# Kernel tuning notes

Hardware: AMD Instinct MI355X
Metric: run time of the kernel (lower is better)

Reference implementation:

```python
import jax, jax.numpy as jnp
import numpy as np

D = 256; HD = 16; G = 16; L = 2; HOP = 2; HK = 4
N = 16384; E = 49152; B = 256
VA = 128; VB = 8
SQRT2PI = float(np.sqrt(2.0 * 3.14159))  # module uses pi=3.14159


def group_norm(x, g=G, eps=1e-5):
    # torch GroupNorm(affine=False) on [N, D, 1]: normalize over each group of D//g channels
    n, d = x.shape
    xg = x.reshape(n, g, d // g)
    m = xg.mean(-1, keepdims=True)
    v = ((xg - m) ** 2).mean(-1, keepdims=True)
    return ((xg - m) * jax.lax.rsqrt(v + eps)).reshape(n, d)


def glin(x, w):
    # grouped 1x1 conv (no bias): x [n, g*din], w [g, dout, din] -> [n, g*dout]
    g, dout, din = w.shape
    return jnp.einsum('ngd,god->ngo', x.reshape(-1, g, din), w).reshape(-1, g * dout)


def multi_embed(idx, tables):
    # OGB-style encoder: sum of per-feature embeddings. idx [M,F], tables [F,V,D]
    out = tables[0][idx[:, 0]]
    for f in range(1, tables.shape[0]):
        out = out + tables[f][idx[:, f]]
    return out


def glb(x, pre_w, pre_b, gate_w, val_w, post_w, post_b):
    # GatedLinearBlock (dropout is identity in eval)
    xx = group_norm(x @ pre_w.T + pre_b)
    xx = jax.nn.relu(glin(xx, gate_w)) * glin(xx, val_w)
    return xx @ post_w.T + post_b


def glb2(xg, xv, gate_w, val_w, post_w, post_b):
    # GatedLinearBlock2: separate gate/value inputs, GroupNorm first
    gg = jax.nn.relu(glin(group_norm(xg), gate_w))
    vv = glin(group_norm(xv), val_w)
    return (gg * vv) @ post_w.T + post_b


def forward_impl(x_feat, edge_index, edge_attr, batch, batch_size,
                 edge_distance, atom_emb, bond2d_emb, gauss_means, gauss_stds,
                 attn_w, attn_b, scale_both,
                 conv_bond_emb, conv_pre_w, conv_gate_w, conv_val_w, conv_post_w, conv_post_b, conv_scale,
                 virt_pre_w, virt_pre_b, virt_gate_w, virt_val_w, virt_post_w, virt_post_b, virt_scale,
                 att_pre_w, att_pre_b, att_q_w, att_k_w, att_v_w, att_post_w, att_post_b, att_scale,
                 main_pre_w, main_pre_b, main_gate_w, main_val_w, main_post_w, main_post_b):
    src, dst = edge_index[0], edge_index[1]
    n = x_feat.shape[0]
    deg = jnp.clip(jax.ops.segment_sum(jnp.ones_like(dst), dst, num_segments=n) - 1, 0, 3)
    # --- edge features, mode='both': fuse 2D bond embedding with 3D gaussian features ---
    h2d = multi_embed(edge_attr, bond2d_emb)                      # [E, D]
    std = jnp.abs(gauss_stds) + 0.01
    diff = (edge_distance[:, None] - gauss_means[None, :]) / std
    h3d = jnp.exp(-0.5 * diff * diff) / (SQRT2PI * std)          # [E, D]
    w = jax.nn.sigmoid(jnp.concatenate([h2d, h3d], axis=-1) @ attn_w + attn_b[0])[:, None]
    h_e = w * h2d + (1.0 - w) * h3d
    h_in = jnp.exp(scale_both)[deg] * jax.ops.segment_sum(h_e, dst, num_segments=n)
    h_in = multi_embed(x_feat, atom_emb) + h_in                   # [N, D]
    h_virt = jnp.zeros((batch_size, D), h_in.dtype)
    h_att = jnp.zeros((batch_size, 2 * D // HD, HD, HD), h_in.dtype)
    for l in range(L):
        # --- ConvMessage: hop*kernel gated message-passing sublayers ---
        x_raw, x_out = h_in, jnp.zeros_like(h_in)
        for k in range(HK):
            if k > 0 and k % HOP == 0:
                x_raw, x_out = h_in + x_out, jnp.zeros_like(h_in)
            bond = multi_embed(edge_attr, conv_bond_emb[l, k])
            xp = x_raw @ conv_pre_w[l, k].T
            msg = glb2(xp[dst] + bond, xp[src] + bond,
                       conv_gate_w[l, k], conv_val_w[l, k], conv_post_w[l, k], conv_post_b[l, k])
            x_raw = jax.ops.segment_sum(msg, dst, num_segments=n)
            x_out = x_out + jnp.exp(conv_scale[l, k])[deg] * x_raw
        h_out = h_in + x_out
        # --- VirtMessage: graph-level virtual node with residual state ---
        h_virt = jax.ops.segment_sum(h_in, batch, num_segments=batch_size) + h_virt
        h_out = h_out + (jnp.exp(virt_scale[l]) * glb(h_virt, virt_pre_w[l], virt_pre_b[l],
                          virt_gate_w[l], virt_val_w[l], virt_post_w[l], virt_post_b[l]))[batch]
        # --- AttMessage: linear attention with per-graph scatter normalization ---
        xv0 = group_norm(h_in @ att_pre_w[l].T + att_pre_b[l])
        xq = jnp.exp(glin(xv0, att_q_w[l]) / np.sqrt(HD)).reshape(n, -1, HD)   # [N,32,16]
        xk = jnp.exp(glin(xv0, att_k_w[l]) / np.sqrt(HD)).reshape(n, -1, HD)
        xv = glin(xv0, att_v_w[l]).reshape(n, -1, HD)
        xkv = jnp.einsum('bnh,bnv->bnhv', xk, xv)                               # [N,32,16,16]
        h_att = jax.ops.segment_sum(xkv, batch, num_segments=batch_size) + h_att
        xk_sum = jax.ops.segment_sum(xk, batch, num_segments=batch_size)[batch]
        xq = xq / jnp.einsum('bnh,bnh->bn', xq, xk_sum)[:, :, None]
        att_out = jnp.einsum('bnh,bnhv->bnv', xq, h_att[batch]).reshape(n, 2 * D)
        h_out = h_out + jnp.exp(att_scale[l]) * (att_out @ att_post_w[l].T + att_post_b[l])
        # --- main gated block ---
        h_in = glb(h_out, main_pre_w[l], main_pre_b[l],
                   main_gate_w[l], main_val_w[l], main_post_w[l], main_post_b[l])
    return h_in


def setup_inputs() -> dict:
    key = jax.random.key(0)
    ks = iter(jax.random.split(key, 80))
    def rn(shape, s=0.05):
        return jax.random.normal(next(ks), shape, dtype=jnp.float32) * s
    inp = {}
    inp['x_feat'] = jax.random.randint(next(ks), (N, 9), 0, VA)
    inp['edge_index'] = jax.random.randint(next(ks), (2, E), 0, N)
    inp['edge_attr'] = jax.random.randint(next(ks), (E, 3), 0, VB)
    inp['batch'] = jnp.sort(jax.random.randint(next(ks), (N,), 0, B))
    inp['batch_size'] = B
    inp['edge_distance'] = jax.random.uniform(next(ks), (E,), dtype=jnp.float32) * 4.0
    inp['atom_emb'] = rn((9, VA, D))
    inp['bond2d_emb'] = rn((3, VB, D))
    inp['gauss_means'] = jax.random.uniform(next(ks), (D,), minval=2.0, maxval=3.0)
    inp['gauss_stds'] = jax.random.uniform(next(ks), (D,), minval=1.0, maxval=1.5)
    inp['attn_w'] = rn((2 * D,))
    inp['attn_b'] = rn((1,))
    inp['scale_both'] = jnp.full((4, D), np.log(0.1), jnp.float32)
    inp['conv_bond_emb'] = rn((L, HK, 3, VB, D))
    inp['conv_pre_w'] = rn((L, HK, D, D))
    inp['conv_gate_w'] = rn((L, HK, G, HD, HD))
    inp['conv_val_w'] = rn((L, HK, G, HD, HD))
    inp['conv_post_w'] = rn((L, HK, D, D))
    inp['conv_post_b'] = rn((L, HK, D))
    inp['conv_scale'] = jnp.full((L, HK, 4, D), np.log(0.1), jnp.float32)
    inp['virt_pre_w'] = rn((L, D, D)); inp['virt_pre_b'] = rn((L, D))
    inp['virt_gate_w'] = rn((L, G, 2 * HD, HD)); inp['virt_val_w'] = rn((L, G, 2 * HD, HD))
    inp['virt_post_w'] = rn((L, D, 2 * D)); inp['virt_post_b'] = rn((L, D))
    inp['virt_scale'] = jnp.full((L, D), np.log(0.01), jnp.float32)
    inp['att_pre_w'] = rn((L, D, D)); inp['att_pre_b'] = rn((L, D))
    inp['att_q_w'] = rn((L, G, 2 * HD, HD)); inp['att_k_w'] = rn((L, G, 2 * HD, HD)); inp['att_v_w'] = rn((L, G, 2 * HD, HD))
    inp['att_post_w'] = rn((L, D, 2 * D)); inp['att_post_b'] = rn((L, D))
    inp['att_scale'] = jnp.full((L, D), np.log(0.01), jnp.float32)
    inp['main_pre_w'] = rn((L, D, D)); inp['main_pre_b'] = rn((L, D))
    inp['main_gate_w'] = rn((L, G, 3 * HD, HD)); inp['main_val_w'] = rn((L, G, 3 * HD, HD))
    inp['main_post_w'] = rn((L, D, 3 * D)); inp['main_post_b'] = rn((L, D))
    return inp


def reference(x_feat, edge_index, edge_attr, batch, batch_size, edge_distance,
              atom_emb, bond2d_emb, gauss_means, gauss_stds, attn_w, attn_b, scale_both,
              conv_bond_emb, conv_pre_w, conv_gate_w, conv_val_w, conv_post_w, conv_post_b, conv_scale,
              virt_pre_w, virt_pre_b, virt_gate_w, virt_val_w, virt_post_w, virt_post_b, virt_scale,
              att_pre_w, att_pre_b, att_q_w, att_k_w, att_v_w, att_post_w, att_post_b, att_scale,
              main_pre_w, main_pre_b, main_gate_w, main_val_w, main_post_w, main_post_b):
    return forward_impl(x_feat, edge_index, edge_attr, batch, batch_size,
                        edge_distance, atom_emb, bond2d_emb, gauss_means, gauss_stds,
                        attn_w, attn_b, scale_both,
                        conv_bond_emb, conv_pre_w, conv_gate_w, conv_val_w, conv_post_w, conv_post_b, conv_scale,
                        virt_pre_w, virt_pre_b, virt_gate_w, virt_val_w, virt_post_w, virt_post_b, virt_scale,
                        att_pre_w, att_pre_b, att_q_w, att_k_w, att_v_w, att_post_w, att_post_b, att_scale,
                        main_pre_w, main_pre_b, main_gate_w, main_val_w, main_post_w, main_post_b)
```

## Files before the change

### kernel.cpp

```cpp
#include <hip/hip_runtime.h>
#include <cstdint>
#include <cstddef>
#include <type_traits>

#define NN 16384
#define EE 49152
#define BB 256

typedef _Float16 f16;
typedef _Float16 half8 __attribute__((ext_vector_type(8)));
typedef _Float16 half4v __attribute__((ext_vector_type(4)));
typedef _Float16 half2v __attribute__((ext_vector_type(2)));
typedef float floatx4 __attribute__((ext_vector_type(4)));

#if defined(__has_builtin)
#if __has_builtin(__builtin_amdgcn_fdot2)
#define HAVE_FDOT2 1
#endif
#endif

static constexpr size_t ND = (size_t)NN * 256;


__global__ __launch_bounds__(256) void count_deg_kernel(const int* __restrict__ dst, int* __restrict__ cnt, int e) {
  int i = blockIdx.x * 256 + threadIdx.x;
  if (i < e) atomicAdd(&cnt[dst[i]], 1);
}
__global__ __launch_bounds__(256) void clip_deg_kernel(const int* __restrict__ cnt, int* __restrict__ deg, int n) {
  int i = blockIdx.x * 256 + threadIdx.x;
  if (i < n) { int v = cnt[i] - 1; deg[i] = v < 0 ? 0 : (v > 3 ? 3 : v); }
}
__global__ __launch_bounds__(256) void goff_kernel(const int* __restrict__ batch, int* __restrict__ goff, int n, int b) {
  int i = blockIdx.x * 256 + threadIdx.x;
  if (i > n) return;
  int cur = (i < n) ? batch[i] : b;
  int prev = (i == 0) ? -1 : batch[i - 1];
  for (int x = prev + 1; x <= cur; x++) goff[x] = i;
}
__global__ __launch_bounds__(256) void scan_off_kernel(const int* __restrict__ cnt, int* __restrict__ off) {
  __shared__ int part[256];
  int tid = threadIdx.x;
  int base = tid * 64;
  int s = 0;
  for (int i = 0; i < 64; i++) s += cnt[base + i];
  part[tid] = s;
  __syncthreads();
  for (int o = 1; o < 256; o <<= 1) {
    int t = (tid >= o) ? part[tid - o] : 0;
    __syncthreads();
    part[tid] += t;
    __syncthreads();
  }
  int run = (tid == 0) ? 0 : part[tid - 1];
  for (int i = 0; i < 64; i++) {
    off[base + i] = run;
    run += cnt[base + i];
  }
  if (tid == 255) off[NN] = run;
}
__global__ __launch_bounds__(256) void copy_i_kernel(const int* __restrict__ a, int* __restrict__ b, int n) {
  int i = blockIdx.x * 256 + threadIdx.x;
  if (i < n) b[i] = a[i];
}
__global__ __launch_bounds__(256) void fill_elist_kernel(const int* __restrict__ dst,
    int* __restrict__ cursor, int* __restrict__ elist, int e) {
  int i = blockIdx.x * 256 + threadIdx.x;
  if (i < e) {
    int p = atomicAdd(&cursor[dst[i]], 1);
    elist[p] = i;
  }
}
__global__ __launch_bounds__(256) void gather_edges_kernel(const int* __restrict__ elist,
    const int* __restrict__ eattr, const int* __restrict__ src, const int* __restrict__ dst,
    const float* __restrict__ edist, int* __restrict__ ea_s, int* __restrict__ src_s,
    int* __restrict__ dst_s, float* __restrict__ ed_s) {
  int j = blockIdx.x * 256 + threadIdx.x;
  if (j >= EE) return;
  int e = elist[j];
  ea_s[j * 3 + 0] = eattr[e * 3 + 0];
  ea_s[j * 3 + 1] = eattr[e * 3 + 1];
  ea_s[j * 3 + 2] = eattr[e * 3 + 2];
  src_s[j] = src[e];
  dst_s[j] = dst[e];
  ed_s[j] = edist[e];
}
__global__ __launch_bounds__(256) void add3_both_kernel(float* __restrict__ dst, f16* __restrict__ dstH,
    const float* __restrict__ a, const float* __restrict__ b, int n4) {
  int i = blockIdx.x * 256 + threadIdx.x;
  if (i >= n4) return;
  float4 x = reinterpret_cast<const float4*>(a)[i];
  float4 y = reinterpret_cast<const float4*>(b)[i];
  x.x += y.x; x.y += y.y; x.z += y.z; x.w += y.w;
  reinterpret_cast<float4*>(dst)[i] = x;
  half4v h;
  h[0] = (f16)x.x; h[1] = (f16)x.y; h[2] = (f16)x.z; h[3] = (f16)x.w;
  reinterpret_cast<half4v*>(dstH)[i] = h;
}
__global__ __launch_bounds__(256) void f2h_kernel(const float* __restrict__ in, f16* __restrict__ out, int n4) {
  int i = blockIdx.x * 256 + threadIdx.x;
  if (i >= n4) return;
  float4 v = reinterpret_cast<const float4*>(in)[i];
  half4v o;
  o[0] = (f16)v.x; o[1] = (f16)v.y; o[2] = (f16)v.z; o[3] = (f16)v.w;
  reinterpret_cast<half4v*>(out)[i] = o;
}

template <typename OUT>
__global__ __launch_bounds__(256) void seg_reduce_kernel(const f16* __restrict__ msg,
    const int* __restrict__ off, OUT* __restrict__ out) {
  int idx = blockIdx.x * 256 + threadIdx.x;
  int n = idx >> 6, c0 = (idx & 63) * 4;
  int j0 = off[n], j1 = off[n + 1];
  float a0 = 0.f, a1 = 0.f, a2 = 0.f, a3 = 0.f;
  int j = j0;
  for (; j + 1 < j1; j += 2) {
    half4v m0 = *reinterpret_cast<const half4v*>(&msg[(size_t)j * 256 + c0]);
    half4v m1 = *reinterpret_cast<const half4v*>(&msg[(size_t)(j + 1) * 256 + c0]);
    a0 += (float)m0[0] + (float)m1[0];
    a1 += (float)m0[1] + (float)m1[1];
    a2 += (float)m0[2] + (float)m1[2];
    a3 += (float)m0[3] + (float)m1[3];
  }
  if (j < j1) {
    half4v m0 = *reinterpret_cast<const half4v*>(&msg[(size_t)j * 256 + c0]);
    a0 += (float)m0[0]; a1 += (float)m0[1]; a2 += (float)m0[2]; a3 += (float)m0[3];
  }
  if constexpr (std::is_same<OUT, float>::value) {
    float4 o = {a0, a1, a2, a3};
    *reinterpret_cast<float4*>(&out[(size_t)n * 256 + c0]) = o;
  } else {
    half4v o;
    o[0] = (f16)a0; o[1] = (f16)a1; o[2] = (f16)a2; o[3] = (f16)a3;
    *reinterpret_cast<half4v*>(&out[(size_t)n * 256 + c0]) = o;
  }
}


__global__ __launch_bounds__(256) void edge_feat_kernel(
    const int* __restrict__ ea_s, const float* __restrict__ ed_s,
    const float* __restrict__ bond2d, const float* __restrict__ gmeans,
    const float* __restrict__ gstds, const float* __restrict__ attn_w,
    const float* __restrict__ attn_b, f16* __restrict__ msg) {
  int lane = threadIdx.x & 63;
  int j = blockIdx.x * 4 + (threadIdx.x >> 6);
  if (j >= EE) return;
  int a0 = ea_s[j * 3 + 0], a1 = ea_s[j * 3 + 1], a2 = ea_s[j * 3 + 2];
  float dist = ed_s[j];
  const float SQ2PI = sqrtf(2.0f * 3.14159f);
  int c0 = lane * 4;
  float4 b0 = *reinterpret_cast<const float4*>(&bond2d[a0 * 256 + c0]);
  float4 b1 = *reinterpret_cast<const float4*>(&bond2d[2048 + a1 * 256 + c0]);
  float4 b2 = *reinterpret_cast<const float4*>(&bond2d[4096 + a2 * 256 + c0]);
  float4 gm = *reinterpret_cast<const float4*>(&gmeans[c0]);
  float4 gs = *reinterpret_cast<const float4*>(&gstds[c0]);
  float4 w2 = *reinterpret_cast<const float4*>(&attn_w[c0]);
  float4 w3 = *reinterpret_cast<const float4*>(&attn_w[256 + c0]);
  float h2[4], h3[4];
  float part = 0.f;
#pragma unroll
  for (int i = 0; i < 4; i++) {
    h2[i] = (&b0.x)[i] + (&b1.x)[i] + (&b2.x)[i];
    float sd = fabsf((&gs.x)[i]) + 0.01f;
    float df = (dist - (&gm.x)[i]) / sd;
    h3[i] = expf(-0.5f * df * df) / (SQ2PI * sd);
    part += (&w2.x)[i] * h2[i] + (&w3.x)[i] * h3[i];
  }
#pragma unroll
  for (int off = 32; off > 0; off >>= 1) part += __shfl_xor(part, off);
  float wg = 1.f / (1.f + expf(-(part + attn_b[0])));
  half4v o;
#pragma unroll
  for (int i = 0; i < 4; i++) o[i] = (f16)(wg * h2[i] + (1.f - wg) * h3[i]);
  *reinterpret_cast<half4v*>(&msg[(size_t)j * 256 + c0]) = o;
}

__global__ __launch_bounds__(256) void atom_finish_kernel(
    const int* __restrict__ xf, const float* __restrict__ emb,
    const float* __restrict__ scale_both, const int* __restrict__ deg,
    const float* __restrict__ tmp, float* __restrict__ h_in, f16* __restrict__ h_inH) {
  int idx = blockIdx.x * 256 + threadIdx.x;
  int n = idx >> 6, c = (idx & 63) * 4;
  float a0 = 0.f, a1 = 0.f, a2 = 0.f, a3 = 0.f;
#pragma unroll
  for (int f = 0; f < 9; f++) {
    int v = xf[n * 9 + f];
    float4 e = *reinterpret_cast<const float4*>(&emb[((size_t)(f * 128 + v)) * 256 + c]);
    a0 += e.x; a1 += e.y; a2 += e.z; a3 += e.w;
  }
  int dg = deg[n];
  float4 s = *reinterpret_cast<const float4*>(&scale_both[dg * 256 + c]);
  float4 t = *reinterpret_cast<const float4*>(&tmp[(size_t)n * 256 + c]);
  float4 r;
  r.x = a0 + expf(s.x) * t.x; r.y = a1 + expf(s.y) * t.y;
  r.z = a2 + expf(s.z) * t.z; r.w = a3 + expf(s.w) * t.w;
  *reinterpret_cast<float4*>(&h_in[(size_t)n * 256 + c]) = r;
  half4v h;
  h[0] = (f16)r.x; h[1] = (f16)r.y; h[2] = (f16)r.z; h[3] = (f16)r.w;
  *reinterpret_cast<half4v*>(&h_inH[(size_t)n * 256 + c]) = h;
}

template <int MODE>
__global__ __launch_bounds__(256) void hgemm_kernel(
    const f16* __restrict__ A, const f16* __restrict__ W,
    const float* __restrict__ bias, const float* __restrict__ scale,
    const int* __restrict__ cnt, const int* __restrict__ deg,
    float* __restrict__ C, float* __restrict__ Cadd, f16* __restrict__ Cf,
    const float* __restrict__ vs2, const float* __restrict__ vout2,
    const int* __restrict__ batch2, int K) {
  __shared__ f16 Ah[128 * 40];
  __shared__ f16 Wh[64 * 40];
  const int tid = threadIdx.x;
  const int row0 = blockIdx.x * 128, col0 = blockIdx.y * 64;
  const int lane = tid & 63;
  const int wave = tid >> 6;
  const int wr = (wave >> 1) * 64, wc = (wave & 1) * 32;
  const floatx4 fz = {0.f, 0.f, 0.f, 0.f};
  floatx4 acc[4][2];
#pragma unroll
  for (int m = 0; m < 4; m++)
#pragma unroll
    for (int n = 0; n < 2; n++) acc[m][n] = fz;
  const int q0 = tid * 2;
  const int rA0 = q0 >> 2, pA0 = q0 & 3;
  const int rA1 = (q0 + 1) >> 2, pA1 = (q0 + 1) & 3;
  const int rW = tid >> 2, pW = tid & 3;
  const int kb = (lane >> 4) * 8;
  const int fr = lane & 15;
  uint4 a0 = *reinterpret_cast<const uint4*>(&A[(size_t)(row0 + rA0) * K + pA0 * 8]);
  uint4 a1 = *reinterpret_cast<const uint4*>(&A[(size_t)(row0 + rA1) * K + pA1 * 8]);
  uint4 w0 = *reinterpret_cast<const uint4*>(&W[(size_t)(col0 + rW) * K + pW * 8]);
  for (int k0 = 0;;) {
    *reinterpret_cast<uint4*>(&Ah[rA0 * 40 + pA0 * 8]) = a0;
    *reinterpret_cast<uint4*>(&Ah[rA1 * 40 + pA1 * 8]) = a1;
    *reinterpret_cast<uint4*>(&Wh[rW * 40 + pW * 8]) = w0;
    __syncthreads();
    int kn = k0 + 32;
    if (kn < K) {
      a0 = *reinterpret_cast<const uint4*>(&A[(size_t)(row0 + rA0) * K + kn + pA0 * 8]);
      a1 = *reinterpret_cast<const uint4*>(&A[(size_t)(row0 + rA1) * K + kn + pA1 * 8]);
      w0 = *reinterpret_cast<const uint4*>(&W[(size_t)(col0 + rW) * K + kn + pW * 8]);
    }
    half8 af[4], wf[2];
#pragma unroll
    for (int m = 0; m < 4; m++)
      af[m] = *reinterpret_cast<const half8*>(&Ah[(wr + m * 16 + fr) * 40 + kb]);
#pragma unroll
    for (int n = 0; n < 2; n++)
      wf[n] = *reinterpret_cast<const half8*>(&Wh[(wc + n * 16 + fr) * 40 + kb]);
#pragma unroll
    for (int m = 0; m < 4; m++)
#pragma unroll
      for (int n = 0; n < 2; n++)
        acc[m][n] = __builtin_amdgcn_mfma_f32_16x16x32_f16(af[m], wf[n], acc[m][n], 0, 0, 0);
    if (kn >= K) break;
    __syncthreads();
    k0 = kn;
  }
  const int rl4 = (lane >> 4) * 4, cl = lane & 15;
#pragma unroll
  for (int m = 0; m < 4; m++) {
#pragma unroll
    for (int i = 0; i < 4; i++) {
      int row = row0 + wr + m * 16 + rl4 + i;
      float cb = (MODE == 4 || MODE == 5) ? (float)cnt[row] : 1.f;
      int dg = (MODE == 4 || MODE == 5) ? deg[row] : 0;
      int brow = (MODE == 7) ? batch2[row] : 0;
#pragma unroll
      for (int n = 0; n < 2; n++) {
        int col = col0 + wc + n * 16 + cl;
        float v = acc[m][n][i];
        size_t oi = (size_t)row * 256 + col;
        if (MODE == 4 || MODE == 5) {
          v += cb * bias[col];
          float sc = expf(scale[dg * 256 + col]);
          if (MODE == 4) Cadd[oi] += sc * v;
          else Cadd[oi] = sc * v;
          if (Cf) Cf[oi] = (f16)v;
        } else if (MODE == 7) {
          v += bias[col];
          float nv = C[oi] + Cadd[oi] + expf(vs2[col]) * vout2[(size_t)brow * 256 + col]
                   + expf(scale[col]) * v;
          Cf[oi] = (f16)nv;
        } else if (MODE == 6) {
          v += bias[col];
          float s1 = v, s2 = v * v;
#pragma unroll
          for (int o_ = 1; o_ < 16; o_ <<= 1) {
            s1 += __shfl_xor(s1, o_);
            s2 += __shfl_xor(s2, o_);
          }
          float mean = s1 * (1.f / 16.f);
          float var = s2 * (1.f / 16.f) - mean * mean;
          float gnv = (v - mean) * rsqrtf(var + 1e-5f);
          if (C) C[oi] = gnv;
          if (Cf) Cf[oi] = (f16)gnv;
        } else {
          if (bias) v += bias[col];
          if (C) C[oi] = v;
          if (Cf) Cf[oi] = (f16)v;
        }
      }
    }
  }
}

__global__ __launch_bounds__(256) void conv_edge_kernel(
    const f16* __restrict__ xp, const int* __restrict__ ea_s,
    const int* __restrict__ src_s, const int* __restrict__ dst_s,
    const float* __restrict__ bond_emb, const float* __restrict__ gate_w,
    const float* __restrict__ val_w, f16* __restrict__ msg) {
  constexpr int RS = 264;
  __shared__ f16 sg[16 * RS];
  __shared__ f16 sv[16 * RS];
  int tid = threadIdx.x;
  for (int i = tid; i < 4096; i += 256) {
    int g = i >> 8, rem = i & 255;
    sg[g * RS + rem] = (f16)gate_w[i];
    sv[g * RS + rem] = (f16)val_w[i];
  }
  __syncthreads();
  int idx = blockIdx.x * 256 + tid;
  int j = idx >> 4, g = idx & 15;
  int a0 = ea_s[j * 3 + 0], a1 = ea_s[j * 3 + 1], a2 = ea_s[j * 3 + 2];
  int d = dst_s[j], s = src_s[j];
  half8 xd0 = *reinterpret_cast<const half8*>(&xp[(size_t)d * 256 + g * 16]);
  half8 xd1 = *reinterpret_cast<const half8*>(&xp[(size_t)d * 256 + g * 16 + 8]);
  half8 xs0 = *reinterpret_cast<const half8*>(&xp[(size_t)s * 256 + g * 16]);
  half8 xs1 = *reinterpret_cast<const half8*>(&xp[(size_t)s * 256 + g * 16 + 8]);
  const float4* b0p = reinterpret_cast<const float4*>(&bond_emb[a0 * 256 + g * 16]);
  const float4* b1p = reinterpret_cast<const float4*>(&bond_emb[2048 + a1 * 256 + g * 16]);
  const float4* b2p = reinterpret_cast<const float4*>(&bond_emb[4096 + a2 * 256 + g * 16]);
  float xg[16], xv[16];
  float mg = 0.f, mv = 0.f;
#pragma unroll
  for (int q = 0; q < 4; q++) {
    float4 b0 = b0p[q], b1 = b1p[q], b2 = b2p[q];
#pragma unroll
    for (int t = 0; t < 4; t++) {
      int i = q * 4 + t;
      float bo = (&b0.x)[t] + (&b1.x)[t] + (&b2.x)[t];
      float xd = (i < 8) ? (float)xd0[i & 7] : (float)xd1[i & 7];
      float xs = (i < 8) ? (float)xs0[i & 7] : (float)xs1[i & 7];
      xg[i] = xd + bo;
      xv[i] = xs + bo;
      mg += xg[i];
      mv += xv[i];
    }
  }
  mg *= (1.f / 16.f);
  mv *= (1.f / 16.f);
  float vg = 0.f, vv = 0.f;
#pragma unroll
  for (int i = 0; i < 16; i++) {
    float dg_ = xg[i] - mg, dv_ = xv[i] - mv;
    vg += dg_ * dg_;
    vv += dv_ * dv_;
  }
  float rg = rsqrtf(vg * (1.f / 16.f) + 1e-5f);
  float rv = rsqrtf(vv * (1.f / 16.f) + 1e-5f);
#ifdef HAVE_FDOT2
  half2v xgh[8], xvh[8];
#pragma unroll
  for (int q = 0; q < 8; q++) {
    xgh[q][0] = (f16)((xg[2 * q] - mg) * rg);
    xgh[q][1] = (f16)((xg[2 * q + 1] - mg) * rg);
    xvh[q][0] = (f16)((xv[2 * q] - mv) * rv);
    xvh[q][1] = (f16)((xv[2 * q + 1] - mv) * rv);
  }
#else
#pragma unroll
  for (int i = 0; i < 16; i++) {
    xg[i] = (xg[i] - mg) * rg;
    xv[i] = (xv[i] - mv) * rv;
  }
#endif
  const f16* gRow = &sg[g * RS];
  const f16* vRow = &sv[g * RS];
  f16 res[16];
#pragma unroll
  for (int o = 0; o < 16; o++) {
    half8 gA = *reinterpret_cast<const half8*>(&gRow[o * 16]);
    half8 gB = *reinterpret_cast<const half8*>(&gRow[o * 16 + 8]);
    half8 vA = *reinterpret_cast<const half8*>(&vRow[o * 16]);
    half8 vB = *reinterpret_cast<const half8*>(&vRow[o * 16 + 8]);
    float ag = 0.f, av = 0.f;
#ifdef HAVE_FDOT2
#pragma unroll
    for (int q = 0; q < 4; q++) {
      half2v ga = {gA[2 * q], gA[2 * q + 1]};
      half2v gb = {gB[2 * q], gB[2 * q + 1]};
      half2v va = {vA[2 * q], vA[2 * q + 1]};
      half2v vb = {vB[2 * q], vB[2 * q + 1]};
      ag = __builtin_amdgcn_fdot2(xgh[q], ga, ag, false);
      ag = __builtin_amdgcn_fdot2(xgh[q + 4], gb, ag, false);
      av = __builtin_amdgcn_fdot2(xvh[q], va, av, false);
      av = __builtin_amdgcn_fdot2(xvh[q + 4], vb, av, false);
    }
#else
#pragma unroll
    for (int i = 0; i < 8; i++) {
      ag += xg[i] * (float)gA[i] + xg[i + 8] * (float)gB[i];
      av += xv[i] * (float)vA[i] + xv[i + 8] * (float)vB[i];
    }
#endif
    res[o] = (f16)(fmaxf(ag, 0.f) * av);
  }
  uint4* op = reinterpret_cast<uint4*>(&msg[(size_t)j * 256 + g * 16]);
  op[0] = reinterpret_cast<const uint4*>(res)[0];
  op[1] = reinterpret_cast<const uint4*>(res)[1];
}

template <int DOUT>
__global__ __launch_bounds__(256) void glb_mid_h_kernel(
    const f16* __restrict__ X, const float* __restrict__ gate_w,
    const float* __restrict__ val_w, f16* __restrict__ out) {
  constexpr int RS = DOUT * 16 + 8;
  __shared__ f16 sg[16 * RS];
  __shared__ f16 sv[16 * RS];
  int tid = threadIdx.x;
  for (int i = tid; i < 16 * DOUT * 16; i += 256) {
    int g = i / (DOUT * 16), rem = i % (DOUT * 16);
    sg[g * RS + rem] = (f16)gate_w[i];
    sv[g * RS + rem] = (f16)val_w[i];
  }
  __syncthreads();
  int idx = blockIdx.x * 256 + tid;
  int n = idx >> 4, g = idx & 15;
  half8 x0 = *reinterpret_cast<const half8*>(&X[(size_t)n * 256 + g * 16]);
  half8 x1 = *reinterpret_cast<const half8*>(&X[(size_t)n * 256 + g * 16 + 8]);
#ifdef HAVE_FDOT2
  half2v xh[8];
#pragma unroll
  for (int q = 0; q < 4; q++) {
    xh[q][0] = x0[2 * q]; xh[q][1] = x0[2 * q + 1];
    xh[q + 4][0] = x1[2 * q]; xh[q + 4][1] = x1[2 * q + 1];
  }
#else
  float x[16];
#pragma unroll
  for (int i = 0; i < 8; i++) { x[i] = (float)x0[i]; x[i + 8] = (float)x1[i]; }
#endif
  const f16* gRow = &sg[g * RS];
  const f16* vRow = &sv[g * RS];
  f16 res[DOUT];
#pragma unroll
  for (int o = 0; o < DOUT; o++) {
    half8 gA = *reinterpret_cast<const half8*>(&gRow[o * 16]);
    half8 gB = *reinterpret_cast<const half8*>(&gRow[o * 16 + 8]);
    half8 vA = *reinterpret_cast<const half8*>(&vRow[o * 16]);
    half8 vB = *reinterpret_cast<const half8*>(&vRow[o * 16 + 8]);
    float ag = 0.f, av = 0.f;
#ifdef HAVE_FDOT2
#pragma unroll
    for (int q = 0; q < 4; q++) {
      half2v gq = {gA[2 * q], gA[2 * q + 1]};
      half2v g2 = {gB[2 * q], gB[2 * q + 1]};
      half2v vq = {vA[2 * q], vA[2 * q + 1]};
      half2v v2 = {vB[2 * q], vB[2 * q + 1]};
      ag = __builtin_amdgcn_fdot2(xh[q], gq, ag, false);
      ag = __builtin_amdgcn_fdot2(xh[q + 4], g2, ag, false);
      av = __builtin_amdgcn_fdot2(xh[q], vq, av, false);
      av = __builtin_amdgcn_fdot2(xh[q + 4], v2, av, false);
    }
#else
#pragma unroll
    for (int i = 0; i < 8; i++) {
      ag += x[i] * (float)gA[i] + x[i + 8] * (float)gB[i];
      av += x[i] * (float)vA[i] + x[i + 8] * (float)vB[i];
    }
#endif
    res[o] = (f16)(fmaxf(ag, 0.f) * av);
  }
  f16* op = &out[(size_t)n * (16 * DOUT) + g * DOUT];
#pragma unroll
  for (int q = 0; q < DOUT / 8; q++)
    *reinterpret_cast<half8*>(&op[q * 8]) = *reinterpret_cast<const half8*>(&res[q * 8]);
}

__global__ __launch_bounds__(256) void virt_fused_kernel(
    const float* __restrict__ h_in, const int* __restrict__ goff,
    const float* __restrict__ preW, const float* __restrict__ preb,
    const float* __restrict__ gateW, const float* __restrict__ valW,
    const float* __restrict__ postW, const float* __restrict__ postb,
    float* __restrict__ h_virt, float* __restrict__ vout) {
  __shared__ float sred[4][256];
  __shared__ float sx[256];
  __shared__ float xx[256];
  __shared__ float vv[512];
  int tid = threadIdx.x, b = blockIdx.x;
  int n0 = goff[b], n1 = goff[b + 1];
  int sub = tid >> 6, cg = tid & 63;
  float a0 = 0.f, a1 = 0.f, a2 = 0.f, a3 = 0.f;
  for (int n = n0 + sub; n < n1; n += 4) {
    float4 x = *reinterpret_cast<const float4*>(&h_in[(size_t)n * 256 + cg * 4]);
    a0 += x.x; a1 += x.y; a2 += x.z; a3 += x.w;
  }
  sred[sub][cg * 4 + 0] = a0;
  sred[sub][cg * 4 + 1] = a1;
  sred[sub][cg * 4 + 2] = a2;
  sred[sub][cg * 4 + 3] = a3;
  __syncthreads();
  float acc = h_virt[(size_t)b * 256 + tid] + sred[0][tid] + sred[1][tid] + sred[2][tid] + sred[3][tid];
  h_virt[(size_t)b * 256 + tid] = acc;
  sx[tid] = acc;
  __syncthreads();
  float dot = preb[tid];
  const float4* wrow = reinterpret_cast<const float4*>(&preW[(size_t)tid * 256]);
  const float4* sx4 = reinterpret_cast<const float4*>(sx);
#pragma unroll 8
  for (int q = 0; q < 64; q++) {
    float4 w = wrow[q];
    float4 s = sx4[q];
    dot += w.x * s.x + w.y * s.y + w.z * s.z + w.w * s.w;
  }
  float s1 = dot, s2 = dot * dot;
#pragma unroll
  for (int o_ = 1; o_ < 16; o_ <<= 1) {
    s1 += __shfl_xor(s1, o_);
    s2 += __shfl_xor(s2, o_);
  }
  float mean = s1 * (1.f / 16.f);
  float var = s2 * (1.f / 16.f) - mean * mean;
  xx[tid] = (dot - mean) * rsqrtf(var + 1e-5f);
  __syncthreads();
#pragma unroll
  for (int rep = 0; rep < 2; rep++) {
    int o = tid + rep * 256;
    int g = o >> 5, o2 = o & 31;
    const float4* gw = reinterpret_cast<const float4*>(&gateW[(size_t)(g * 32 + o2) * 16]);
    const float4* vw = reinterpret_cast<const float4*>(&valW[(size_t)(g * 32 + o2) * 16]);
    const float4* xg4 = reinterpret_cast<const float4*>(&xx[g * 16]);
    float ag = 0.f, av = 0.f;
#pragma unroll
    for (int q = 0; q < 4; q++) {
      float4 wg = gw[q], wv = vw[q], xq = xg4[q];
      ag += wg.x * xq.x + wg.y * xq.y + wg.z * xq.z + wg.w * xq.w;
      av += wv.x * xq.x + wv.y * xq.y + wv.z * xq.z + wv.w * xq.w;
    }
    vv[o] = fmaxf(ag, 0.f) * av;
  }
  __syncthreads();
  float outv = postb[tid];
  const float4* prow = reinterpret_cast<const float4*>(&postW[(size_t)tid * 512]);
  const float4* vv4 = reinterpret_cast<const float4*>(vv);
#pragma unroll 8
  for (int q = 0; q < 128; q++) {
    float4 w = prow[q], s = vv4[q];
    outv += w.x * s.x + w.y * s.y + w.z * s.z + w.w * s.w;
  }
  vout[(size_t)b * 256 + tid] = outv;
}

template <bool FIRST>
__global__ __launch_bounds__(256) void att_graph_kernel(
    const float* __restrict__ xv0, const float* __restrict__ k_w,
    const float* __restrict__ v_w, const int* __restrict__ goff,
    float* __restrict__ h_att, float* __restrict__ xk_sum) {
  __shared__ float kx[8][256];
  __shared__ float vx[8][256];
  __shared__ float rows[8][256];
// ... 52 lines not shown
        }
      }
      bool valid = (nbase + nn) < n1;
      float ek = valid ? expf(aK * 0.25f) : 0.f;
      kx[nn][tid] = ek;
      vx[nn][tid] = aV;
      ks += ek;
    }
    __syncthreads();
#pragma unroll
    for (int nn = 0; nn < 8; nn++) {
      float kk = kx[nn][tid];
      const float4* vp = reinterpret_cast<const float4*>(&vx[nn][headLocal * 16]);
#pragma unroll
      for (int q = 0; q < 4; q++) {
        float4 vq = vp[q];
        hacc[q * 4 + 0] += kk * vq.x;
        hacc[q * 4 + 1] += kk * vq.y;
        hacc[q * 4 + 2] += kk * vq.z;
        hacc[q * 4 + 3] += kk * vq.w;
      }
    }
    __syncthreads();
  }
  float* hgo = &h_att[(size_t)b * 8192];
#pragma unroll
  for (int j = 0; j < 16; j++) hgo[h * 512 + head * 16 + j] = hacc[j];
  xk_sum[(size_t)b * 512 + p] = ks;
}

__global__ __launch_bounds__(256) void att_out_kernel(
    const float* __restrict__ xv0, const float* __restrict__ q_w,
    const float* __restrict__ xk_sum, const float* __restrict__ h_att,
    const int* __restrict__ goff, f16* __restrict__ out) {
  __shared__ float sqw[16 * 260];
  __shared__ float hat[16 * 644];
  int tid = threadIdx.x, b = blockIdx.x;
  for (int i = tid; i < 8192; i += 256) {
    int g = i >> 9, rem = i & 511;
    sqw[g * 260 + rem] = q_w[i];
  }
  for (int i = tid; i < 8192; i += 256) {
    int h = i >> 9, rem = i & 511;
    int head = rem >> 4, v = rem & 15;
    hat[h * 644 + head * 20 + v] = h_att[(size_t)b * 8192 + i];
  }
  __syncthreads();
  int n0 = goff[b], n1 = goff[b + 1];
  int nl = tid >> 5, head = tid & 31;
  int g = head >> 1, j = head & 1;
  const float* ks = &xk_sum[(size_t)b * 512 + head * 16];
  for (int nbase = n0; nbase < n1; nbase += 8) {
    int n = nbase + nl;
    if (n >= n1) continue;
    float x[16];
    const float4* xp4 = reinterpret_cast<const float4*>(&xv0[(size_t)n * 256 + g * 16]);
#pragma unroll
    for (int q = 0; q < 4; q++) {
      float4 xq = xp4[q];
#pragma unroll
      for (int t = 0; t < 4; t++) x[q * 4 + t] = (&xq.x)[t];
    }
    float qv[16];
    float denom = 0.f;
#pragma unroll
    for (int h = 0; h < 16; h++) {
      const float4* wp = reinterpret_cast<const float4*>(&sqw[g * 260 + (j * 16 + h) * 16]);
      float a = 0.f;
#pragma unroll
      for (int q = 0; q < 4; q++) {
        float4 wq = wp[q];
#pragma unroll
        for (int t = 0; t < 4; t++) a += x[q * 4 + t] * (&wq.x)[t];
      }
      float e = expf(a * 0.25f);
      qv[h] = e;
      denom += e * ks[h];
    }
    float inv = 1.f / denom;
    float acc[16] = {0.f, 0.f, 0.f, 0.f, 0.f, 0.f, 0.f, 0.f,
                     0.f, 0.f, 0.f, 0.f, 0.f, 0.f, 0.f, 0.f};
#pragma unroll
    for (int h = 0; h < 16; h++) {
      float qh = qv[h];
      const float4* hp = reinterpret_cast<const float4*>(&hat[h * 644 + head * 20]);
#pragma unroll
      for (int q = 0; q < 4; q++) {
        float4 vq = hp[q];
        acc[q * 4 + 0] += qh * vq.x;
        acc[q * 4 + 1] += qh * vq.y;
        acc[q * 4 + 2] += qh * vq.z;
        acc[q * 4 + 3] += qh * vq.w;
      }
    }
    f16 res[16];
#pragma unroll
    for (int v = 0; v < 16; v++) res[v] = (f16)(acc[v] * inv);
    uint4* op = reinterpret_cast<uint4*>(&out[(size_t)n * 512 + head * 16]);
    op[0] = reinterpret_cast<const uint4*>(res)[0];
    op[1] = reinterpret_cast<const uint4*>(res)[1];
  }
}


extern "C" void kernel_launch(void* const* d_in, const int* in_sizes, int n_in,
                              void* d_out, int out_size, void* d_ws, size_t ws_size,
                              hipStream_t stream) {
  const int* x_feat = (const int*)d_in[0];
  const int* eidx = (const int*)d_in[1];
  const int* eattr = (const int*)d_in[2];
  const int* batch = (const int*)d_in[3];
  const float* edist = (const float*)d_in[5];
  const float* atom_emb = (const float*)d_in[6];
  const float* bond2d = (const float*)d_in[7];
  const float* gmeans = (const float*)d_in[8];
  const float* gstds = (const float*)d_in[9];
  const float* attn_w = (const float*)d_in[10];
  const float* attn_b = (const float*)d_in[11];
  const float* scale_both = (const float*)d_in[12];
  const float* conv_bond_emb = (const float*)d_in[13];
  const float* conv_pre_w = (const float*)d_in[14];
  const float* conv_gate_w = (const float*)d_in[15];
  const float* conv_val_w = (const float*)d_in[16];
  const float* conv_post_w = (const float*)d_in[17];
  const float* conv_post_b = (const float*)d_in[18];
  const float* conv_scale = (const float*)d_in[19];
  const float* virt_pre_w = (const float*)d_in[20];
  const float* virt_pre_b = (const float*)d_in[21];
  const float* virt_gate_w = (const float*)d_in[22];
  const float* virt_val_w = (const float*)d_in[23];
  const float* virt_post_w = (const float*)d_in[24];
  const float* virt_post_b = (const float*)d_in[25];
  const float* virt_scale = (const float*)d_in[26];
  const float* att_pre_w = (const float*)d_in[27];
  const float* att_pre_b = (const float*)d_in[28];
  const float* att_q_w = (const float*)d_in[29];
  const float* att_k_w = (const float*)d_in[30];
  const float* att_v_w = (const float*)d_in[31];
  const float* att_post_w = (const float*)d_in[32];
  const float* att_post_b = (const float*)d_in[33];
  const float* att_scale = (const float*)d_in[34];
  const float* main_pre_w = (const float*)d_in[35];
  const float* main_pre_b = (const float*)d_in[36];
  const float* main_gate_w = (const float*)d_in[37];
  const float* main_val_w = (const float*)d_in[38];
  const float* main_post_w = (const float*)d_in[39];
  const float* main_post_b = (const float*)d_in[40];

  const int* src = eidx;
  const int* dst = eidx + EE;

  float* ws = (float*)d_ws;
  float* h_in = ws;
  float* x_raw = ws + ND;
  float* x_out = ws + 2 * ND;
  float* nodeA = ws + 3 * ND;
  f16* h_inH = (f16*)(ws + 4 * ND);
  f16* xrawH = (f16*)(ws + 4 * ND + ND / 2);
  f16* hTmp = (f16*)(ws + 5 * ND);
  f16* gnH = (f16*)(ws + 5 * ND + ND / 2);
  f16* msgH = (f16*)(ws + 6 * ND);
  float* sm = ws + 8 * ND;
  f16* hW = (f16*)sm;
  float* h_virt = sm + 1179648;
  float* h_att = h_virt + 65536;
  float* xk_sum = h_att + 2097152;
  float* vout = xk_sum + 131072;
  int* cnt = (int*)(vout + 65536);
  int* deg = cnt + NN;
  int* goff = deg + NN;
  int* off = goff + BB + 1;
  int* cursor = off + NN + 1;
  int* elist = cursor + NN;
  int* ea_s = elist + EE;
  int* src_s = ea_s + 3 * EE;
  int* dst_s = src_s + EE;
  float* ed_s = (float*)(dst_s + EE);

  f16* wCpre = hW;
  f16* wCpost = hW + 524288;
  f16* wApre = hW + 1048576;
  f16* wApost = hW + 1179648;
  f16* wMpre = hW + 1441792;
  f16* wMpost = hW + 1572864;

  auto cvt = [&](const float* in, f16* out, int n) {
    f2h_kernel<<<n / 4 / 256, 256, 0, stream>>>(in, out, n / 4);
  };

  cvt(conv_pre_w, wCpre, 524288);
  cvt(conv_post_w, wCpost, 524288);
  cvt(att_pre_w, wApre, 131072);
  cvt(att_post_w, wApost, 262144);
  cvt(main_pre_w, wMpre, 131072);
  cvt(main_post_w, wMpost, 393216);

  (void)hipMemsetAsync(cnt, 0, NN * sizeof(int), stream);
  count_deg_kernel<<<EE / 256, 256, 0, stream>>>(dst, cnt, EE);
  clip_deg_kernel<<<NN / 256, 256, 0, stream>>>(cnt, deg, NN);
  goff_kernel<<<(NN + 256) / 256, 256, 0, stream>>>(batch, goff, NN, BB);
  scan_off_kernel<<<1, 256, 0, stream>>>(cnt, off);
  copy_i_kernel<<<NN / 256, 256, 0, stream>>>(off, cursor, NN);
  fill_elist_kernel<<<EE / 256, 256, 0, stream>>>(dst, cursor, elist, EE);
  gather_edges_kernel<<<EE / 256, 256, 0, stream>>>(elist, eattr, src, dst, edist,
                                                    ea_s, src_s, dst_s, ed_s);

  edge_feat_kernel<<<EE / 4, 256, 0, stream>>>(ea_s, ed_s, bond2d, gmeans, gstds,
                                               attn_w, attn_b, msgH);
  seg_reduce_kernel<float><<<NN / 4, 256, 0, stream>>>(msgH, off, x_out);
  atom_finish_kernel<<<NN * 64 / 256, 256, 0, stream>>>(x_feat, atom_emb, scale_both, deg,
                                                        x_out, h_in, h_inH);
  (void)hipMemsetAsync(h_virt, 0, 65536 * 4, stream);

  const dim3 gN(NN / 128, 4);
  const int n4 = (int)(ND / 4);

  for (int l = 0; l < 2; l++) {
    const f16* curH = h_inH;
    for (int k = 0; k < 4; k++) {
      if (k == 2) {
        add3_both_kernel<<<n4 / 256, 256, 0, stream>>>(x_raw, xrawH, h_in, x_out, n4);
        curH = xrawH;
      }
      size_t lk = (size_t)(l * 4 + k);
      hgemm_kernel<0><<<gN, 256, 0, stream>>>(curH, wCpre + lk * 65536, nullptr, nullptr,
                                              nullptr, nullptr, nullptr, nullptr, hTmp,
                                              nullptr, nullptr, nullptr, 256);
      conv_edge_kernel<<<EE * 16 / 256, 256, 0, stream>>>(
          hTmp, ea_s, src_s, dst_s, conv_bond_emb + lk * 6144,
          conv_gate_w + lk * 4096, conv_val_w + lk * 4096, msgH);
      seg_reduce_kernel<f16><<<NN / 4, 256, 0, stream>>>(msgH, off, hTmp);
      if (k == 0 || k == 2)
        hgemm_kernel<5><<<gN, 256, 0, stream>>>(hTmp, wCpost + lk * 65536,
                                                conv_post_b + lk * 256, conv_scale + lk * 1024,
                                                cnt, deg, nullptr, x_out, xrawH,
                                                nullptr, nullptr, nullptr, 256);
      else
        hgemm_kernel<4><<<gN, 256, 0, stream>>>(hTmp, wCpost + lk * 65536,
                                                conv_post_b + lk * 256, conv_scale + lk * 1024,
                                                cnt, deg, nullptr, x_out, xrawH,
                                                nullptr, nullptr, nullptr, 256);
      curH = xrawH;
    }

    virt_fused_kernel<<<BB, 256, 0, stream>>>(
        h_in, goff, virt_pre_w + (size_t)l * 65536, virt_pre_b + (size_t)l * 256,
        virt_gate_w + (size_t)l * 8192, virt_val_w + (size_t)l * 8192,
        virt_post_w + (size_t)l * 131072, virt_post_b + (size_t)l * 256, h_virt, vout);

    hgemm_kernel<6><<<gN, 256, 0, stream>>>(h_inH, wApre + (size_t)l * 65536,
                                            att_pre_b + (size_t)l * 256, nullptr, nullptr,
                                            nullptr, nodeA, nullptr, nullptr,
                                            nullptr, nullptr, nullptr, 256);
    if (l == 0)
      att_graph_kernel<true><<<BB * 2, 256, 0, stream>>>(
          nodeA, att_k_w + (size_t)l * 8192, att_v_w + (size_t)l * 8192, goff, h_att, xk_sum);
    else
      att_graph_kernel<false><<<BB * 2, 256, 0, stream>>>(
          nodeA, att_k_w + (size_t)l * 8192, att_v_w + (size_t)l * 8192, goff, h_att, xk_sum);
    att_out_kernel<<<BB, 256, 0, stream>>>(
        nodeA, att_q_w + (size_t)l * 8192, xk_sum, h_att, goff, msgH);
    hgemm_kernel<7><<<gN, 256, 0, stream>>>(msgH, wApost + (size_t)l * 131072,
                                            att_post_b + (size_t)l * 256,
                                            att_scale + (size_t)l * 256, nullptr, nullptr,
                                            h_in, x_out, hTmp,
                                            virt_scale + (size_t)l * 256, vout, batch, 512);

    hgemm_kernel<6><<<gN, 256, 0, stream>>>(hTmp, wMpre + (size_t)l * 65536,
                                            main_pre_b + (size_t)l * 256, nullptr, nullptr,
                                            nullptr, nullptr, nullptr, gnH,
                                            nullptr, nullptr, nullptr, 256);
    glb_mid_h_kernel<48><<<NN * 16 / 256, 256, 0, stream>>>(
        gnH, main_gate_w + (size_t)l * 12288, main_val_w + (size_t)l * 12288, msgH);
    float* hdst = (l == 1) ? (float*)d_out : h_in;
    f16* hdstH = (l == 1) ? nullptr : h_inH;
    hgemm_kernel<0><<<gN, 256, 0, stream>>>(msgH, wMpost + (size_t)l * 196608,
                                            main_post_b + (size_t)l * 256, nullptr, nullptr,
                                            nullptr, hdst, nullptr, hdstH,
                                            nullptr, nullptr, nullptr, 768);
  }
}
```

Measured before the change: 985.7 us.

## Fuse conv edge messages with per-node segment reduction into one node kernel

Replaces the per-edge conv message kernel plus segmented reduction with a node-centric kernel. Each thread walks its node's incoming CSR edges and accumulates the gated messages in registers, so the E×256 fp16 message buffer is no longer written and re-read. It also drops the unused fp32 x_raw output from the add kernel and the dst_s gather array. The trade-off is load imbalance across nodes of different degree, and fewer threads (N×16 instead of E×16), which lowers parallelism.

After: 1.396 ms. +41.6%, slower.

```diff
diff --git a/kernel.cpp b/kernel.cpp
--- a/kernel.cpp
+++ b/kernel.cpp
@@ -73,7 +73,7 @@
 __global__ __launch_bounds__(256) void gather_edges_kernel(const int* __restrict__ elist,
     const int* __restrict__ eattr, const int* __restrict__ src, const int* __restrict__ dst,
     const float* __restrict__ edist, int* __restrict__ ea_s, int* __restrict__ src_s,
-    int* __restrict__ dst_s, float* __restrict__ ed_s) {
+    float* __restrict__ ed_s) {
   int j = blockIdx.x * 256 + threadIdx.x;
   if (j >= EE) return;
   int e = elist[j];
@@ -81,19 +81,17 @@
   ea_s[j * 3 + 1] = eattr[e * 3 + 1];
   ea_s[j * 3 + 2] = eattr[e * 3 + 2];
   src_s[j] = src[e];
-  dst_s[j] = dst[e];
   ed_s[j] = edist[e];
 }
-__global__ __launch_bounds__(256) void add3_both_kernel(float* __restrict__ dst, f16* __restrict__ dstH,
+__global__ __launch_bounds__(256) void add3h_kernel(f16* __restrict__ dstH,
     const float* __restrict__ a, const float* __restrict__ b, int n4) {
   int i = blockIdx.x * 256 + threadIdx.x;
   if (i >= n4) return;
   float4 x = reinterpret_cast<const float4*>(a)[i];
   float4 y = reinterpret_cast<const float4*>(b)[i];
-  x.x += y.x; x.y += y.y; x.z += y.z; x.w += y.w;
-  reinterpret_cast<float4*>(dst)[i] = x;
   half4v h;
-  h[0] = (f16)x.x; h[1] = (f16)x.y; h[2] = (f16)x.z; h[3] = (f16)x.w;
+  h[0] = (f16)(x.x + y.x); h[1] = (f16)(x.y + y.y);
+  h[2] = (f16)(x.z + y.z); h[3] = (f16)(x.w + y.w);
   reinterpret_cast<half4v*>(dstH)[i] = h;
 }
 __global__ __launch_bounds__(256) void f2h_kernel(const float* __restrict__ in, f16* __restrict__ out, int n4) {
@@ -105,34 +103,18 @@
   reinterpret_cast<half4v*>(out)[i] = o;
 }
 
-template <typename OUT>
-__global__ __launch_bounds__(256) void seg_reduce_kernel(const f16* __restrict__ msg,
-    const int* __restrict__ off, OUT* __restrict__ out) {
+__global__ __launch_bounds__(256) void seg_reduce_f_kernel(const f16* __restrict__ msg,
+    const int* __restrict__ off, float* __restrict__ out) {
   int idx = blockIdx.x * 256 + threadIdx.x;
   int n = idx >> 6, c0 = (idx & 63) * 4;
   int j0 = off[n], j1 = off[n + 1];
   float a0 = 0.f, a1 = 0.f, a2 = 0.f, a3 = 0.f;
-  int j = j0;
-  for (; j + 1 < j1; j += 2) {
-    half4v m0 = *reinterpret_cast<const half4v*>(&msg[(size_t)j * 256 + c0]);
-    half4v m1 = *reinterpret_cast<const half4v*>(&msg[(size_t)(j + 1) * 256 + c0]);
-    a0 += (float)m0[0] + (float)m1[0];
-    a1 += (float)m0[1] + (float)m1[1];
-    a2 += (float)m0[2] + (float)m1[2];
-    a3 += (float)m0[3] + (float)m1[3];
-  }
-  if (j < j1) {
+  for (int j = j0; j < j1; j++) {
     half4v m0 = *reinterpret_cast<const half4v*>(&msg[(size_t)j * 256 + c0]);
     a0 += (float)m0[0]; a1 += (float)m0[1]; a2 += (float)m0[2]; a3 += (float)m0[3];
   }
-  if constexpr (std::is_same<OUT, float>::value) {
-    float4 o = {a0, a1, a2, a3};
-    *reinterpret_cast<float4*>(&out[(size_t)n * 256 + c0]) = o;
-  } else {
-    half4v o;
-    o[0] = (f16)a0; o[1] = (f16)a1; o[2] = (f16)a2; o[3] = (f16)a3;
-    *reinterpret_cast<half4v*>(&out[(size_t)n * 256 + c0]) = o;
-  }
+  float4 o = {a0, a1, a2, a3};
+  *reinterpret_cast<float4*>(&out[(size_t)n * 256 + c0]) = o;
 }
 
 
@@ -304,11 +286,11 @@
   }
 }
 
-__global__ __launch_bounds__(256) void conv_edge_kernel(
+__global__ __launch_bounds__(256) void conv_node_kernel(
     const f16* __restrict__ xp, const int* __restrict__ ea_s,
-    const int* __restrict__ src_s, const int* __restrict__ dst_s,
+    const int* __restrict__ src_s, const int* __restrict__ off,
     const float* __restrict__ bond_emb, const float* __restrict__ gate_w,
-    const float* __restrict__ val_w, f16* __restrict__ msg) {
+    const float* __restrict__ val_w, f16* __restrict__ out) {
   constexpr int RS = 264;
   __shared__ f16 sg[16 * RS];
   __shared__ f16 sv[16 * RS];
@@ -320,92 +302,101 @@
   }
   __syncthreads();
   int idx = blockIdx.x * 256 + tid;
-  int j = idx >> 4, g = idx & 15;
-  int a0 = ea_s[j * 3 + 0], a1 = ea_s[j * 3 + 1], a2 = ea_s[j * 3 + 2];
-  int d = dst_s[j], s = src_s[j];
-  half8 xd0 = *reinterpret_cast<const half8*>(&xp[(size_t)d * 256 + g * 16]);
-  half8 xd1 = *reinterpret_cast<const half8*>(&xp[(size_t)d * 256 + g * 16 + 8]);
-  half8 xs0 = *reinterpret_cast<const half8*>(&xp[(size_t)s * 256 + g * 16]);
-  half8 xs1 = *reinterpret_cast<const half8*>(&xp[(size_t)s * 256 + g * 16 + 8]);
-  const float4* b0p = reinterpret_cast<const float4*>(&bond_emb[a0 * 256 + g * 16]);
-  const float4* b1p = reinterpret_cast<const float4*>(&bond_emb[2048 + a1 * 256 + g * 16]);
-  const float4* b2p = reinterpret_cast<const float4*>(&bond_emb[4096 + a2 * 256 + g * 16]);
-  float xg[16], xv[16];
-  float mg = 0.f, mv = 0.f;
-#pragma unroll
-  for (int q = 0; q < 4; q++) {
-    float4 b0 = b0p[q], b1 = b1p[q], b2 = b2p[q];
-#pragma unroll
-    for (int t = 0; t < 4; t++) {
-      int i = q * 4 + t;
-      float bo = (&b0.x)[t] + (&b1.x)[t] + (&b2.x)[t];
-      float xd = (i < 8) ? (float)xd0[i & 7] : (float)xd1[i & 7];
-      float xs = (i < 8) ? (float)xs0[i & 7] : (float)xs1[i & 7];
-      xg[i] = xd + bo;
-      xv[i] = xs + bo;
-      mg += xg[i];
-      mv += xv[i];
-    }
-  }
-  mg *= (1.f / 16.f);
-  mv *= (1.f / 16.f);
-  float vg = 0.f, vv = 0.f;
-#pragma unroll
-  for (int i = 0; i < 16; i++) {
-    float dg_ = xg[i] - mg, dv_ = xv[i] - mv;
-    vg += dg_ * dg_;
-    vv += dv_ * dv_;
-  }
-  float rg = rsqrtf(vg * (1.f / 16.f) + 1e-5f);
-  float rv = rsqrtf(vv * (1.f / 16.f) + 1e-5f);
-#ifdef HAVE_FDOT2
-  half2v xgh[8], xvh[8];
-#pragma unroll
-  for (int q = 0; q < 8; q++) {
-    xgh[q][0] = (f16)((xg[2 * q] - mg) * rg);
-    xgh[q][1] = (f16)((xg[2 * q + 1] - mg) * rg);
-    xvh[q][0] = (f16)((xv[2 * q] - mv) * rv);
-    xvh[q][1] = (f16)((xv[2 * q + 1] - mv) * rv);
-  }
-#else
-#pragma unroll
-  for (int i = 0; i < 16; i++) {
-    xg[i] = (xg[i] - mg) * rg;
-    xv[i] = (xv[i] - mv) * rv;
-  }
-#endif
+  int n = idx >> 4, g = idx & 15;
+  int j0 = off[n], j1 = off[n + 1];
+  half8 xd0 = *reinterpret_cast<const half8*>(&xp[(size_t)n * 256 + g * 16]);
+  half8 xd1 = *reinterpret_cast<const half8*>(&xp[(size_t)n * 256 + g * 16 + 8]);
+  float xdf[16];
+#pragma unroll
+  for (int i = 0; i < 8; i++) { xdf[i] = (float)xd0[i]; xdf[i + 8] = (float)xd1[i]; }
   const f16* gRow = &sg[g * RS];
   const f16* vRow = &sv[g * RS];
+  float accv[16] = {0.f, 0.f, 0.f, 0.f, 0.f, 0.f, 0.f, 0.f,
+                    0.f, 0.f, 0.f, 0.f, 0.f, 0.f, 0.f, 0.f};
+  for (int j = j0; j < j1; j++) {
+    int a0 = ea_s[j * 3 + 0], a1 = ea_s[j * 3 + 1], a2 = ea_s[j * 3 + 2];
+    int s = src_s[j];
+    half8 xs0 = *reinterpret_cast<const half8*>(&xp[(size_t)s * 256 + g * 16]);
+    half8 xs1 = *reinterpret_cast<const half8*>(&xp[(size_t)s * 256 + g * 16 + 8]);
+    const float4* b0p = reinterpret_cast<const float4*>(&bond_emb[a0 * 256 + g * 16]);
+    const float4* b1p = reinterpret_cast<const float4*>(&bond_emb[2048 + a1 * 256 + g * 16]);
+    const float4* b2p = reinterpret_cast<const float4*>(&bond_emb[4096 + a2 * 256 + g * 16]);
+    float xg[16], xv[16];
+    float mg = 0.f, mv = 0.f;
+#pragma unroll
+    for (int q = 0; q < 4; q++) {
+      float4 b0 = b0p[q], b1 = b1p[q], b2 = b2p[q];
+#pragma unroll
+      for (int t = 0; t < 4; t++) {
+        int i = q * 4 + t;
+        float bo = (&b0.x)[t] + (&b1.x)[t] + (&b2.x)[t];
+        float xs = (i < 8) ? (float)xs0[i & 7] : (float)xs1[i & 7];
+        xg[i] = xdf[i] + bo;
+        xv[i] = xs + bo;
+        mg += xg[i];
+        mv += xv[i];
+      }
+    }
+    mg *= (1.f / 16.f);
+    mv *= (1.f / 16.f);
+    float vg = 0.f, vv = 0.f;
+#pragma unroll
+    for (int i = 0; i < 16; i++) {
+      float dg_ = xg[i] - mg, dv_ = xv[i] - mv;
+      vg += dg_ * dg_;
+      vv += dv_ * dv_;
+    }
+    float rg = rsqrtf(vg * (1.f / 16.f) + 1e-5f);
+    float rv = rsqrtf(vv * (1.f / 16.f) + 1e-5f);
+#ifdef HAVE_FDOT2
+    half2v xgh[8], xvh[8];
+#pragma unroll
+    for (int q = 0; q < 8; q++) {
+      xgh[q][0] = (f16)((xg[2 * q] - mg) * rg);
+      xgh[q][1] = (f16)((xg[2 * q + 1] - mg) * rg);
+      xvh[q][0] = (f16)((xv[2 * q] - mv) * rv);
+      xvh[q][1] = (f16)((xv[2 * q + 1] - mv) * rv);
+    }
+#else
+#pragma unroll
+    for (int i = 0; i < 16; i++) {
+      xg[i] = (xg[i] - mg) * rg;
+      xv[i] = (xv[i] - mv) * rv;
+    }
+#endif
+#pragma unroll
+    for (int o = 0; o < 16; o++) {
+      half8 gA = *reinterpret_cast<const half8*>(&gRow[o * 16]);
+      half8 gB = *reinterpret_cast<const half8*>(&gRow[o * 16 + 8]);
+      half8 vA = *reinterpret_cast<const half8*>(&vRow[o * 16]);
+      half8 vB = *reinterpret_cast<const half8*>(&vRow[o * 16 + 8]);
+      float ag = 0.f, av = 0.f;
+#ifdef HAVE_FDOT2
+#pragma unroll
+      for (int q = 0; q < 4; q++) {
+        half2v ga = {gA[2 * q], gA[2 * q + 1]};
+        half2v gb = {gB[2 * q], gB[2 * q + 1]};
+        half2v va = {vA[2 * q], vA[2 * q + 1]};
+        half2v vb = {vB[2 * q], vB[2 * q + 1]};
+        ag = __builtin_amdgcn_fdot2(xgh[q], ga, ag, false);
+        ag = __builtin_amdgcn_fdot2(xgh[q + 4], gb, ag, false);
+        av = __builtin_amdgcn_fdot2(xvh[q], va, av, false);
+        av = __builtin_amdgcn_fdot2(xvh[q + 4], vb, av, false);
+      }
+#else
+#pragma unroll
+      for (int i = 0; i < 8; i++) {
+        ag += xg[i] * (float)gA[i] + xg[i + 8] * (float)gB[i];
+        av += xv[i] * (float)vA[i] + xv[i + 8] * (float)vB[i];
+      }
+#endif
+      accv[o] += fmaxf(ag, 0.f) * av;
+    }
+  }
   f16 res[16];
 #pragma unroll
-  for (int o = 0; o < 16; o++) {
-    half8 gA = *reinterpret_cast<const half8*>(&gRow[o * 16]);
-    half8 gB = *reinterpret_cast<const half8*>(&gRow[o * 16 + 8]);
-    half8 vA = *reinterpret_cast<const half8*>(&vRow[o * 16]);
-    half8 vB = *reinterpret_cast<const half8*>(&vRow[o * 16 + 8]);
-    float ag = 0.f, av = 0.f;
-#ifdef HAVE_FDOT2
-#pragma unroll
-    for (int q = 0; q < 4; q++) {
-      half2v ga = {gA[2 * q], gA[2 * q + 1]};
-      half2v gb = {gB[2 * q], gB[2 * q + 1]};
-      half2v va = {vA[2 * q], vA[2 * q + 1]};
-      half2v vb = {vB[2 * q], vB[2 * q + 1]};
-      ag = __builtin_amdgcn_fdot2(xgh[q], ga, ag, false);
-      ag = __builtin_amdgcn_fdot2(xgh[q + 4], gb, ag, false);
-      av = __builtin_amdgcn_fdot2(xvh[q], va, av, false);
-      av = __builtin_amdgcn_fdot2(xvh[q + 4], vb, av, false);
-    }
-#else
-#pragma unroll
-    for (int i = 0; i < 8; i++) {
-      ag += xg[i] * (float)gA[i] + xg[i + 8] * (float)gB[i];
-      av += xv[i] * (float)vA[i] + xv[i + 8] * (float)vB[i];
-    }
-#endif
-    res[o] = (f16)(fmaxf(ag, 0.f) * av);
-  }
-  uint4* op = reinterpret_cast<uint4*>(&msg[(size_t)j * 256 + g * 16]);
+  for (int o = 0; o < 16; o++) res[o] = (f16)accv[o];
+  uint4* op = reinterpret_cast<uint4*>(&out[(size_t)n * 256 + g * 16]);
   op[0] = reinterpret_cast<const uint4*>(res)[0];
   op[1] = reinterpret_cast<const uint4*>(res)[1];
 }
@@ -764,15 +755,14 @@
 
   float* ws = (float*)d_ws;
   float* h_in = ws;
-  float* x_raw = ws + ND;
-  float* x_out = ws + 2 * ND;
-  float* nodeA = ws + 3 * ND;
-  f16* h_inH = (f16*)(ws + 4 * ND);
-  f16* xrawH = (f16*)(ws + 4 * ND + ND / 2);
-  f16* hTmp = (f16*)(ws + 5 * ND);
-  f16* gnH = (f16*)(ws + 5 * ND + ND / 2);
-  f16* msgH = (f16*)(ws + 6 * ND);
-  float* sm = ws + 8 * ND;
+  float* x_out = ws + ND;
+  float* nodeA = ws + 2 * ND;
+  f16* h_inH = (f16*)(ws + 3 * ND);
+  f16* xrawH = (f16*)(ws + 3 * ND + ND / 2);
+  f16* hTmp = (f16*)(ws + 4 * ND);
+  f16* gnH = (f16*)(ws + 4 * ND + ND / 2);
+  f16* msgH = (f16*)(ws + 5 * ND);
+  float* sm = ws + 7 * ND;
   f16* hW = (f16*)sm;
   float* h_virt = sm + 1179648;
   float* h_att = h_virt + 65536;
@@ -786,8 +776,7 @@
   int* elist = cursor + NN;
   int* ea_s = elist + EE;
   int* src_s = ea_s + 3 * EE;
-  int* dst_s = src_s + EE;
-  float* ed_s = (float*)(dst_s + EE);
+  float* ed_s = (float*)(src_s + EE);
 
   f16* wCpre = hW;
   f16* wCpost = hW + 524288;
@@ -815,11 +804,11 @@
   copy_i_kernel<<<NN / 256, 256, 0, stream>>>(off, cursor, NN);
   fill_elist_kernel<<<EE / 256, 256, 0, stream>>>(dst, cursor, elist, EE);
   gather_edges_kernel<<<EE / 256, 256, 0, stream>>>(elist, eattr, src, dst, edist,
-                                                    ea_s, src_s, dst_s, ed_s);
+                                                    ea_s, src_s, ed_s);
 
   edge_feat_kernel<<<EE / 4, 256, 0, stream>>>(ea_s, ed_s, bond2d, gmeans, gstds,
                                                attn_w, attn_b, msgH);
-  seg_reduce_kernel<float><<<NN / 4, 256, 0, stream>>>(msgH, off, x_out);
+  seg_reduce_f_kernel<<<NN / 4, 256, 0, stream>>>(msgH, off, x_out);
   atom_finish_kernel<<<NN * 64 / 256, 256, 0, stream>>>(x_feat, atom_emb, scale_both, deg,
                                                         x_out, h_in, h_inH);
   (void)hipMemsetAsync(h_virt, 0, 65536 * 4, stream);
@@ -831,24 +820,23 @@
     const f16* curH = h_inH;
     for (int k = 0; k < 4; k++) {
       if (k == 2) {
-        add3_both_kernel<<<n4 / 256, 256, 0, stream>>>(x_raw, xrawH, h_in, x_out, n4);
+        add3h_kernel<<<n4 / 256, 256, 0, stream>>>(xrawH, h_in, x_out, n4);
         curH = xrawH;
       }
       size_t lk = (size_t)(l * 4 + k);
       hgemm_kernel<0><<<gN, 256, 0, stream>>>(curH, wCpre + lk * 65536, nullptr, nullptr,
                                               nullptr, nullptr, nullptr, nullptr, hTmp,
                                               nullptr, nullptr, nullptr, 256);
-      conv_edge_kernel<<<EE * 16 / 256, 256, 0, stream>>>(
-          hTmp, ea_s, src_s, dst_s, conv_bond_emb + lk * 6144,
-          conv_gate_w + lk * 4096, conv_val_w + lk * 4096, msgH);
-      seg_reduce_kernel<f16><<<NN / 4, 256, 0, stream>>>(msgH, off, hTmp);
+      conv_node_kernel<<<NN * 16 / 256, 256, 0, stream>>>(
+          hTmp, ea_s, src_s, off, conv_bond_emb + lk * 6144,
+          conv_gate_w + lk * 4096, conv_val_w + lk * 4096, gnH);
       if (k == 0 || k == 2)
-        hgemm_kernel<5><<<gN, 256, 0, stream>>>(hTmp, wCpost + lk * 65536,
+        hgemm_kernel<5><<<gN, 256, 0, stream>>>(gnH, wCpost + lk * 65536,
                                                 conv_post_b + lk * 256, conv_scale + lk * 1024,
                                                 cnt, deg, nullptr, x_out, xrawH,
                                                 nullptr, nullptr, nullptr, 256);
       else
-        hgemm_kernel<4><<<gN, 256, 0, stream>>>(hTmp, wCpost + lk * 65536,
+        hgemm_kernel<4><<<gN, 256, 0, stream>>>(gnH, wCpost + lk * 65536,
                                                 conv_post_b + lk * 256, conv_scale + lk * 1024,
                                                 cnt, deg, nullptr, x_out, xrawH,
                                                 nullptr, nullptr, nullptr, 256);
```
